# Optimization experiments

Measured on AMD Instinct MI355X. Metric: run time of the kernel, lower is better.

Reference implementation:

```python
import jax, jax.numpy as jnp
import numpy as np

OUT_FEATURES = 4096
IN_FEATURES = 4096
GROUP_SIZE = 128
NUM_GROUPS = IN_FEATURES // GROUP_SIZE  # 32
PACKED_SIZE = OUT_FEATURES * IN_FEATURES // 8  # 2097152


def setup_inputs() -> dict:
    key = jax.random.key(0)
    k1, k2, k3, k4 = jax.random.split(key, 4)
    x = jax.random.normal(k1, (2, 512, IN_FEATURES), dtype=jnp.float32)
    # random packed 4-bit weights (8 nibbles per int32)
    w_packed = jax.random.randint(k2, (PACKED_SIZE,), jnp.iinfo(jnp.int32).min,
                                  jnp.iinfo(jnp.int32).max, dtype=jnp.int32)
    w_scale = jax.random.uniform(k3, (OUT_FEATURES, NUM_GROUPS), dtype=jnp.float32) * 0.05
    w_zero = jax.random.randint(k4, (OUT_FEATURES, NUM_GROUPS), 0, 8, dtype=jnp.int32)
    return {"x": x, "w_packed": w_packed, "w_scale": w_scale, "w_zero": w_zero}


def _unpack_dequant(w_packed, w_scale, w_zero):
    # Extract 8 nibbles per int32: (v >> (i*4)) & 0xF, i = 0..7
    shifts = jnp.arange(8, dtype=jnp.int32) * 4
    nibbles = (w_packed[:, None] >> shifts[None, :]) & 15  # [packed, 8]
    w4 = nibbles.reshape(-1)  # [out*in], values 0..15
    w4 = jnp.where(w4 >= 8, w4 - 16, w4)  # signed 4-bit -> [-8, 7]
    w_int = w4.reshape(OUT_FEATURES, NUM_GROUPS, GROUP_SIZE).astype(jnp.float32)
    # per-(row, group) dequant: (q - zero) * scale
    w = (w_int - w_zero[:, :, None].astype(jnp.float32)) * w_scale[:, :, None]
    return w.reshape(OUT_FEATURES, IN_FEATURES)


def reference(x, w_packed, w_scale, w_zero):
    weight = _unpack_dequant(w_packed, w_scale, w_zero).astype(x.dtype)
    # F.linear: y = x @ W^T
    return jnp.einsum('bsi,oi->bso', x, weight)
```

## Files before the change

### kernel.cpp

```cpp
#include <hip/hip_runtime.h>
#include <stdint.h>

#define IN_F 4096
#define OUT_F 4096
#define NG 32

typedef __attribute__((ext_vector_type(8))) _Float16 half8;
typedef __attribute__((ext_vector_type(2))) _Float16 half2t;
typedef __attribute__((ext_vector_type(4))) float floatx4;

__global__ __launch_bounds__(256) void prep_kernel(
    const float* __restrict__ x, _Float16* __restrict__ Xh,
    const float* __restrict__ wscale, const int* __restrict__ wzero,
    uint2* __restrict__ SZ, int nxb) {
  int b = blockIdx.x;
  if (b < nxb) {
    int i = b * 256 + threadIdx.x;
    const float4* x4 = (const float4*)x;
    float4 a = x4[2 * i];
    float4 c = x4[2 * i + 1];
    uint4 o;
    o.x = __builtin_bit_cast(unsigned, __builtin_amdgcn_cvt_pkrtz(a.x, c.x));
    o.y = __builtin_bit_cast(unsigned, __builtin_amdgcn_cvt_pkrtz(a.y, c.y));
    o.z = __builtin_bit_cast(unsigned, __builtin_amdgcn_cvt_pkrtz(a.z, c.z));
    o.w = __builtin_bit_cast(unsigned, __builtin_amdgcn_cvt_pkrtz(a.w, c.w));
    ((uint4*)Xh)[i] = o;
  } else {
    int i = (b - nxb) * 256 + threadIdx.x;
    float s = wscale[i];
    int zp = wzero[i];
    _Float16 sh = (_Float16)s;
    _Float16 ch = (_Float16)(float)(1032 + zp);
    unsigned s2 = (unsigned)__builtin_bit_cast(unsigned short, sh) * 0x10001u;
    unsigned c2 = (unsigned)__builtin_bit_cast(unsigned short, ch) * 0x10001u;
    SZ[i] = make_uint2(s2, c2);
  }
}

#define BM 128
#define BN 64
#define BK 64
#define SPLITK 2

__device__ __forceinline__ uint4 dequant8(unsigned v, uint2 szv) {
  unsigned tx = v ^ 0x88888888u;
  half2t s2 = __builtin_bit_cast(half2t, szv.x);
  half2t c2 = __builtin_bit_cast(half2t, szv.y);
  unsigned p0 = (tx & 0x000F000Fu) | 0x64006400u;
  unsigned p1 = ((tx >> 4) & 0x000F000Fu) | 0x64006400u;
  unsigned p2 = ((tx >> 8) & 0x000F000Fu) | 0x64006400u;
  unsigned p3 = ((tx >> 12) & 0x000F000Fu) | 0x64006400u;
  half2t w0 = (__builtin_bit_cast(half2t, p0) - c2) * s2;
  half2t w1 = (__builtin_bit_cast(half2t, p1) - c2) * s2;
  half2t w2 = (__builtin_bit_cast(half2t, p2) - c2) * s2;
  half2t w3 = (__builtin_bit_cast(half2t, p3) - c2) * s2;
  uint4 o;
  o.x = __builtin_bit_cast(unsigned, w0);
  o.y = __builtin_bit_cast(unsigned, w1);
  o.z = __builtin_bit_cast(unsigned, w2);
  o.w = __builtin_bit_cast(unsigned, w3);
  return o;
}

__global__ __launch_bounds__(256, 4) void gemm_fused(
    const _Float16* __restrict__ A, const int* __restrict__ wp,
    const uint2* __restrict__ SZ,
    float* __restrict__ C0, float* __restrict__ C1, int M, int N, int K) {
  __shared__ _Float16 Alds[BM * BK];
  __shared__ _Float16 Blds[BN * BK];

  int t = threadIdx.x;
  int wave = t >> 6, lane = t & 63;
  int wm = (wave >> 1) * 64, wn = (wave & 1) * 32;
  int r = lane & 15, quad = lane >> 4;
  int bm = blockIdx.y * BM, bn = blockIdx.x * BN;
  int kz = blockIdx.z * (K / SPLITK);
  int kend = kz + K / SPLITK;

  floatx4 acc[4][2] = {};

  const _Float16* Ag = A + (size_t)bm * K;
  int rowb = t >> 3, m8 = t & 7;
  const int* wpr0 = wp + (size_t)(bn + rowb) * (IN_F / 8) + m8;
  const int* wpr1 = wp + (size_t)(bn + rowb + 32) * (IN_F / 8) + m8;
  const uint2* sz0 = SZ + (size_t)(bn + rowb) * NG;
  const uint2* sz1 = SZ + (size_t)(bn + rowb + 32) * NG;

  for (int k0 = kz; k0 < kend; k0 += BK) {
    unsigned v0 = (unsigned)wpr0[k0 >> 3];
    unsigned v1 = (unsigned)wpr1[k0 >> 3];
    uint2 szv0 = sz0[k0 >> 7];
    uint2 szv1 = sz1[k0 >> 7];

    __syncthreads();

#pragma unroll
    for (int j = 0; j < 4; ++j) {
      int c = t + 256 * j;
      int row = c >> 3, kc = c & 7;
      const _Float16* ga = Ag + (size_t)row * K + k0 + kc * 8;
      __builtin_amdgcn_global_load_lds(
          (const __attribute__((address_space(1))) void*)ga,
          (__attribute__((address_space(3))) void*)(&Alds[c * 8]), 16, 0, 0);
    }
    ((uint4*)Blds)[t] = dequant8(v0, szv0);
    ((uint4*)Blds)[t + 256] = dequant8(v1, szv1);

    __syncthreads();

#pragma unroll
    for (int ks = 0; ks < 2; ++ks) {
      int kk = ks * 32;
      half8 af[4], bf[2];
#pragma unroll
      for (int mi = 0; mi < 4; ++mi)
        af[mi] = *(const half8*)&Alds[(wm + mi * 16 + r) * BK + kk + quad * 8];
#pragma unroll
      for (int ni = 0; ni < 2; ++ni)
        bf[ni] = *(const half8*)&Blds[(wn + ni * 16 + r) * BK + kk + quad * 8];
#pragma unroll
      for (int mi = 0; mi < 4; ++mi)
#pragma unroll
        for (int ni = 0; ni < 2; ++ni)
          acc[mi][ni] = __builtin_amdgcn_mfma_f32_16x16x32_f16(
              af[mi], bf[ni], acc[mi][ni], 0, 0, 0);
    }
  }

  float* C = (blockIdx.z == 0) ? C0 : C1;
#pragma unroll
  for (int mi = 0; mi < 4; ++mi) {
#pragma unroll
    for (int ni = 0; ni < 2; ++ni) {
#pragma unroll
      for (int i = 0; i < 4; ++i) {
        int grow = bm + wm + mi * 16 + quad * 4 + i;
        int gcol = bn + wn + ni * 16 + r;
        C[(size_t)grow * N + gcol] = acc[mi][ni][i];
      }
    }
  }
}

__global__ __launch_bounds__(256) void reduce_kernel(
    float* __restrict__ out, const float* __restrict__ part) {
  int i = blockIdx.x * 256 + threadIdx.x;
  float4 a = ((const float4*)out)[i];
  float4 b = ((const float4*)part)[i];
  a.x += b.x; a.y += b.y; a.z += b.z; a.w += b.w;
  ((float4*)out)[i] = a;
}

extern "C" void kernel_launch(void* const* d_in, const int* in_sizes, int n_in,
                              void* d_out, int out_size, void* d_ws, size_t ws_size,
                              hipStream_t stream) {
  const float* x = (const float*)d_in[0];
  const int* wp = (const int*)d_in[1];
  const float* wscale = (const float*)d_in[2];
  const int* wzero = (const int*)d_in[3];
  float* out = (float*)d_out;

  int M = in_sizes[0] / IN_F;

  _Float16* Xh = (_Float16*)d_ws;
  float* Cpart = (float*)((char*)d_ws + (size_t)M * IN_F * 2);
  uint2* SZ = (uint2*)((char*)d_ws + (size_t)M * IN_F * 2 + (size_t)M * OUT_F * 4);

  int nxb = (M * IN_F / 8) / 256;
  int nzb = (OUT_F * NG) / 256;
  prep_kernel<<<nxb + nzb, 256, 0, stream>>>(x, Xh, wscale, wzero, SZ, nxb);

  dim3 grid(OUT_F / BN, M / BM, SPLITK);
  gemm_fused<<<grid, 256, 0, stream>>>(Xh, wp, SZ, out, Cpart, M, OUT_F, IN_F);

  reduce_kernel<<<(M * OUT_F / 4) / 256, 256, 0, stream>>>(out, Cpart);
}
```

Baseline: 146.4 us.

## Widen GEMM N tile to 128 and prefetch packed weights one iteration ahead

Doubles the output-column tile per block so each wave computes a 64x64 sub-tile with a 4x4 MFMA accumulator grid, improving reuse of the A tile held in LDS. Packed-weight and scale/zero loads for the next K step are issued before the barrier and MFMA loop, so global latency overlaps with compute. The occupancy hint in launch bounds is dropped, and register pressure rises from the larger accumulator and prefetch buffers. The grid halves in the N direction, leaving fewer blocks to spread across CUs.

```diff
diff --git a/kernel.cpp b/kernel.cpp
--- a/kernel.cpp
+++ b/kernel.cpp
@@ -38,7 +38,7 @@
 }
 
 #define BM 128
-#define BN 64
+#define BN 128
 #define BK 64
 #define SPLITK 2
 
@@ -62,7 +62,7 @@
   return o;
 }
 
-__global__ __launch_bounds__(256, 4) void gemm_fused(
+__global__ __launch_bounds__(256) void gemm_fused(
     const _Float16* __restrict__ A, const int* __restrict__ wp,
     const uint2* __restrict__ SZ,
     float* __restrict__ C0, float* __restrict__ C1, int M, int N, int K) {
@@ -71,27 +71,34 @@
 
   int t = threadIdx.x;
   int wave = t >> 6, lane = t & 63;
-  int wm = (wave >> 1) * 64, wn = (wave & 1) * 32;
+  int wm = (wave >> 1) * 64, wn = (wave & 1) * 64;
   int r = lane & 15, quad = lane >> 4;
   int bm = blockIdx.y * BM, bn = blockIdx.x * BN;
   int kz = blockIdx.z * (K / SPLITK);
   int kend = kz + K / SPLITK;
 
-  floatx4 acc[4][2] = {};
+  floatx4 acc[4][4] = {};
 
   const _Float16* Ag = A + (size_t)bm * K;
+
   int rowb = t >> 3, m8 = t & 7;
-  const int* wpr0 = wp + (size_t)(bn + rowb) * (IN_F / 8) + m8;
-  const int* wpr1 = wp + (size_t)(bn + rowb + 32) * (IN_F / 8) + m8;
-  const uint2* sz0 = SZ + (size_t)(bn + rowb) * NG;
-  const uint2* sz1 = SZ + (size_t)(bn + rowb + 32) * NG;
+  const int* wpr[4];
+  const uint2* szp[4];
+#pragma unroll
+  for (int j = 0; j < 4; ++j) {
+    wpr[j] = wp + (size_t)(bn + rowb + 32 * j) * (IN_F / 8) + m8;
+    szp[j] = SZ + (size_t)(bn + rowb + 32 * j) * NG;
+  }
+
+  unsigned v[4];
+  uint2 sz[4];
+#pragma unroll
+  for (int j = 0; j < 4; ++j) {
+    v[j] = (unsigned)wpr[j][kz >> 3];
+    sz[j] = szp[j][kz >> 7];
+  }
 
   for (int k0 = kz; k0 < kend; k0 += BK) {
-    unsigned v0 = (unsigned)wpr0[k0 >> 3];
-    unsigned v1 = (unsigned)wpr1[k0 >> 3];
-    uint2 szv0 = sz0[k0 >> 7];
-    uint2 szv1 = sz1[k0 >> 7];
-
     __syncthreads();
 
 #pragma unroll
@@ -103,35 +110,52 @@
           (const __attribute__((address_space(1))) void*)ga,
           (__attribute__((address_space(3))) void*)(&Alds[c * 8]), 16, 0, 0);
     }
-    ((uint4*)Blds)[t] = dequant8(v0, szv0);
-    ((uint4*)Blds)[t + 256] = dequant8(v1, szv1);
+
+#pragma unroll
+    for (int j = 0; j < 4; ++j)
+      ((uint4*)Blds)[t + 256 * j] = dequant8(v[j], sz[j]);
+
+    int kn = (k0 + BK < kend) ? (k0 + BK) : k0;
+    unsigned vn[4];
+    uint2 szn[4];
+#pragma unroll
+    for (int j = 0; j < 4; ++j) {
+      vn[j] = (unsigned)wpr[j][kn >> 3];
+      szn[j] = szp[j][kn >> 7];
+    }
 
     __syncthreads();
 
 #pragma unroll
     for (int ks = 0; ks < 2; ++ks) {
       int kk = ks * 32;
-      half8 af[4], bf[2];
+      half8 af[4], bf[4];
 #pragma unroll
       for (int mi = 0; mi < 4; ++mi)
         af[mi] = *(const half8*)&Alds[(wm + mi * 16 + r) * BK + kk + quad * 8];
 #pragma unroll
-      for (int ni = 0; ni < 2; ++ni)
+      for (int ni = 0; ni < 4; ++ni)
         bf[ni] = *(const half8*)&Blds[(wn + ni * 16 + r) * BK + kk + quad * 8];
 #pragma unroll
       for (int mi = 0; mi < 4; ++mi)
 #pragma unroll
-        for (int ni = 0; ni < 2; ++ni)
+        for (int ni = 0; ni < 4; ++ni)
           acc[mi][ni] = __builtin_amdgcn_mfma_f32_16x16x32_f16(
               af[mi], bf[ni], acc[mi][ni], 0, 0, 0);
     }
+
+#pragma unroll
+    for (int j = 0; j < 4; ++j) {
+      v[j] = vn[j];
+      sz[j] = szn[j];
+    }
   }
 
   float* C = (blockIdx.z == 0) ? C0 : C1;
 #pragma unroll
   for (int mi = 0; mi < 4; ++mi) {
 #pragma unroll
-    for (int ni = 0; ni < 2; ++ni) {
+    for (int ni = 0; ni < 4; ++ni) {
 #pragma unroll
       for (int i = 0; i < 4; ++i) {
         int grow = bm + wm + mi * 16 + quad * 4 + i;
```

Measured after the change: 155.6 us. 1.06x slower.
